# Kernel optimization log

Hardware: AMD Instinct MI355X
Metric: run time of the kernel (lower is better)

The kernel has to match this reference:

```python
import jax, jax.numpy as jnp
import numpy as np

N_NODES = 4096
N_EDGES = 131072  # avg degree 32
N_STEPS = 1000


def setup_inputs() -> dict:
    key = jax.random.key(0)
    k1, k2, k3 = jax.random.split(key, 3)
    # Transition matrices: positive entries so the evidence division is well-conditioned.
    Qt = jax.random.uniform(k1, (N_STEPS, 2, 2), minval=0.1, maxval=1.0, dtype=jnp.float32)
    edge_index_x_t = jax.random.randint(k2, (2, N_EDGES), 0, N_NODES)
    edge_index_x_start = jax.random.randint(k3, (2, N_EDGES), 0, N_NODES)
    return {
        "Qt": Qt,
        "edge_index_x_t": edge_index_x_t,
        "edge_index_x_start": edge_index_x_start,
        "t": 500,
        "num_nodes": N_NODES,
    }


def _edge_index_to_adj(edge_index, num_nodes):
    # Dense binary adjacency, matching torch edge_index_to_adj.
    adj = jnp.zeros((num_nodes, num_nodes), dtype=jnp.int32)
    return adj.at[edge_index[0], edge_index[1]].set(1)


def reference(Qt, edge_index_x_t, edge_index_x_start, t, num_nodes):
    # q(x_{t-1} | x_t, x_0) = (Q0[:, x_t] * Q_{t-1}[x_0, :]) / Q_t[x_0, x_t]
    Q_likelihood = Qt[0]        # (2, 2)
    Q_prior = Qt[t - 1]         # (2, 2)  (batch of 1 identical time)
    Q_evidence = Qt[t]          # (2, 2)

    adj_x_t = _edge_index_to_adj(edge_index_x_t, num_nodes)      # (N, N) in {0,1}
    adj_x_start = _edge_index_to_adj(edge_index_x_start, num_nodes)

    # likelihood[i,j,k] = Q_likelihood[k, adj_x_t[i,j]]
    likelihood = jnp.transpose(Q_likelihood[:, adj_x_t], (1, 2, 0))  # (N, N, 2)
    # prior[i,j,:] = Q_prior[adj_x_start[i,j], :]
    prior = Q_prior[adj_x_start]                                     # (N, N, 2)
    # evidence[i,j] = Q_evidence[adj_x_start[i,j], adj_x_t[i,j]]
    evidence = Q_evidence[adj_x_start, adj_x_t][..., None]           # (N, N, 1)

    q_backward = likelihood * prior / evidence                       # (N, N, 2)

    # block_diag of a single triu(N,N,diag=1) mask == upper triangle (all possible edges)
    iu, ju = jnp.triu_indices(num_nodes, k=1)
    # forward returns q_backward_all[:, 1]
    return q_backward[iu, ju, 1]                                     # (N*(N-1)/2,)
```

## Files before the change

kernel.cpp:

```cpp
#include <hip/hip_runtime.h>
#include <cstdint>

#define N_NODES 4096
#define N_EDGES 131072
#define OUT_QUADS (N_NODES * (N_NODES - 1) / 2 / 4)

__device__ __forceinline__ void compute_vals(const float* __restrict__ Qt,
                                             const int* __restrict__ t_ptr,
                                             float* vals) {
    const int t = t_ptr[0];
    const float l0 = Qt[2], l1 = Qt[3];
    const float p0 = Qt[(t - 1) * 4 + 1], p1 = Qt[(t - 1) * 4 + 3];
    const float e00 = Qt[t * 4 + 0], e01 = Qt[t * 4 + 1];
    const float e10 = Qt[t * 4 + 2], e11 = Qt[t * 4 + 3];
    float v0 = l0 * p0 / e00;
    float v1 = l1 * p0 / e01;
    float v2 = l0 * p1 / e10;
    float v3 = l1 * p1 / e11;
    uint32_t u0 = __float_as_uint(v0) & ~1u;
    uint32_t u1 = __float_as_uint(v1) |  1u;
    uint32_t u2 = __float_as_uint(v2) & ~1u;
    uint32_t u3 = __float_as_uint(v3) |  1u;
    vals[0] = __uint_as_float(u0);
    vals[1] = __uint_as_float(u1);
    vals[2] = __uint_as_float(u2);
    vals[3] = __uint_as_float(u3);
}

__device__ __forceinline__ int tri_idx(int i, int j) {
    return i * (2 * N_NODES - i - 1) / 2 + (j - i - 1);
}

__global__ void gt_fill_default(const float* __restrict__ Qt,
                                const int* __restrict__ t_ptr,
                                float4* __restrict__ out) {
    float vals[4];
    compute_vals(Qt, t_ptr, vals);
    const float4 v = make_float4(vals[0], vals[0], vals[0], vals[0]);
    int idx = blockIdx.x * blockDim.x + threadIdx.x;
    out[idx] = v;
}

__global__ void gt_scatter_t(const float* __restrict__ Qt,
                             const int* __restrict__ t_ptr,
                             const int* __restrict__ et,
                             float* __restrict__ out) {
    float vals[4];
    compute_vals(Qt, t_ptr, vals);
    int e = blockIdx.x * blockDim.x + threadIdx.x;
    int i = et[e];
    int j = et[N_EDGES + e];
    if (i < j) out[tri_idx(i, j)] = vals[1];
}

__global__ void gt_scatter_s(const float* __restrict__ Qt,
                             const int* __restrict__ t_ptr,
                             const int* __restrict__ es,
                             float* __restrict__ out) {
    float vals[4];
    compute_vals(Qt, t_ptr, vals);
    int e = blockIdx.x * blockDim.x + threadIdx.x;
    int i = es[e];
    int j = es[N_EDGES + e];
    if (i < j) {
        int idx = tri_idx(i, j);
        uint32_t cur = __float_as_uint(out[idx]);
        out[idx] = (cur & 1u) ? vals[3] : vals[2];
    }
}

extern "C" void kernel_launch(void* const* d_in, const int* in_sizes, int n_in,
                              void* d_out, int out_size, void* d_ws, size_t ws_size,
                              hipStream_t stream) {
    const float* Qt = (const float*)d_in[0];
    const int* et = (const int*)d_in[1];
    const int* es = (const int*)d_in[2];
    const int* t_ptr = (const int*)d_in[3];
    float* out = (float*)d_out;

    gt_fill_default<<<OUT_QUADS / 256, 256, 0, stream>>>(Qt, t_ptr, (float4*)out);
    gt_scatter_t<<<N_EDGES / 256, 256, 0, stream>>>(Qt, t_ptr, et, out);
    gt_scatter_s<<<N_EDGES / 256, 256, 0, stream>>>(Qt, t_ptr, es, out);
}
```

Before: 81.74 us.

## Build adjacency bitmaps with atomics then write output in one dense pass

The old approach filled the whole ~33MB output and then scattered edge values in two passes, the second pass reading back the output. The new version first builds two bitmaps in workspace, one per edge list, using atomicOr over the packed upper-triangle index. A single dense kernel then reads both bitmaps and writes each output quad from the four precomputed values. This drops the random read-modify-write scatters over the output. In exchange it adds a memset, an atomic bitmap pass and a bitmap read.

```diff
diff --git a/kernel.cpp b/kernel.cpp
--- a/kernel.cpp
+++ b/kernel.cpp
@@ -3,7 +3,9 @@
 
 #define N_NODES 4096
 #define N_EDGES 131072
-#define OUT_QUADS (N_NODES * (N_NODES - 1) / 2 / 4)
+#define OUT_ELEMS (N_NODES * (N_NODES - 1) / 2)
+#define OUT_QUADS (OUT_ELEMS / 4)
+#define BM_WORDS_PAD 262144
 
 __device__ __forceinline__ void compute_vals(const float* __restrict__ Qt,
                                              const int* __restrict__ t_ptr,
@@ -13,60 +15,59 @@
     const float p0 = Qt[(t - 1) * 4 + 1], p1 = Qt[(t - 1) * 4 + 3];
     const float e00 = Qt[t * 4 + 0], e01 = Qt[t * 4 + 1];
     const float e10 = Qt[t * 4 + 2], e11 = Qt[t * 4 + 3];
-    float v0 = l0 * p0 / e00;
-    float v1 = l1 * p0 / e01;
-    float v2 = l0 * p1 / e10;
-    float v3 = l1 * p1 / e11;
-    uint32_t u0 = __float_as_uint(v0) & ~1u;
-    uint32_t u1 = __float_as_uint(v1) |  1u;
-    uint32_t u2 = __float_as_uint(v2) & ~1u;
-    uint32_t u3 = __float_as_uint(v3) |  1u;
-    vals[0] = __uint_as_float(u0);
-    vals[1] = __uint_as_float(u1);
-    vals[2] = __uint_as_float(u2);
-    vals[3] = __uint_as_float(u3);
+    vals[0] = l0 * p0 / e00;
+    vals[1] = l1 * p0 / e01;
+    vals[2] = l0 * p1 / e10;
+    vals[3] = l1 * p1 / e11;
 }
 
 __device__ __forceinline__ int tri_idx(int i, int j) {
     return i * (2 * N_NODES - i - 1) / 2 + (j - i - 1);
 }
 
-__global__ void gt_fill_default(const float* __restrict__ Qt,
-                                const int* __restrict__ t_ptr,
-                                float4* __restrict__ out) {
+__global__ void gt_build_bitmaps(const int* __restrict__ et,
+                                 const int* __restrict__ es,
+                                 uint32_t* __restrict__ bm) {
+    int e = blockIdx.x * blockDim.x + threadIdx.x;
+    const int* __restrict__ lst;
+    uint32_t* __restrict__ map;
+    if (e < N_EDGES) {
+        lst = et;
+        map = bm;
+    } else {
+        lst = es;
+        map = bm + BM_WORDS_PAD;
+        e -= N_EDGES;
+    }
+    int i = lst[e];
+    int j = lst[N_EDGES + e];
+    if (i < j) {
+        int k = tri_idx(i, j);
+        atomicOr(&map[k >> 5], 1u << (k & 31));
+    }
+}
+
+__global__ void gt_write(const float* __restrict__ Qt,
+                         const int* __restrict__ t_ptr,
+                         const uint32_t* __restrict__ bm,
+                         float4* __restrict__ out) {
     float vals[4];
     compute_vals(Qt, t_ptr, vals);
-    const float4 v = make_float4(vals[0], vals[0], vals[0], vals[0]);
-    int idx = blockIdx.x * blockDim.x + threadIdx.x;
-    out[idx] = v;
-}
 
-__global__ void gt_scatter_t(const float* __restrict__ Qt,
-                             const int* __restrict__ t_ptr,
-                             const int* __restrict__ et,
-                             float* __restrict__ out) {
-    float vals[4];
-    compute_vals(Qt, t_ptr, vals);
-    int e = blockIdx.x * blockDim.x + threadIdx.x;
-    int i = et[e];
-    int j = et[N_EDGES + e];
-    if (i < j) out[tri_idx(i, j)] = vals[1];
-}
+    int tid = blockIdx.x * blockDim.x + threadIdx.x;
+    int w = tid >> 3;
+    int sh = (tid & 7) * 4;
+    uint32_t wt = bm[w] >> sh;
+    uint32_t ws = bm[BM_WORDS_PAD + w] >> sh;
 
-__global__ void gt_scatter_s(const float* __restrict__ Qt,
-                             const int* __restrict__ t_ptr,
-                             const int* __restrict__ es,
-                             float* __restrict__ out) {
-    float vals[4];
-    compute_vals(Qt, t_ptr, vals);
-    int e = blockIdx.x * blockDim.x + threadIdx.x;
-    int i = es[e];
-    int j = es[N_EDGES + e];
-    if (i < j) {
-        int idx = tri_idx(i, j);
-        uint32_t cur = __float_as_uint(out[idx]);
-        out[idx] = (cur & 1u) ? vals[3] : vals[2];
+    float r[4];
+#pragma unroll
+    for (int k = 0; k < 4; ++k) {
+        bool bt = (wt >> k) & 1u;
+        bool bs = (ws >> k) & 1u;
+        r[k] = bs ? (bt ? vals[3] : vals[2]) : (bt ? vals[1] : vals[0]);
     }
+    out[tid] = make_float4(r[0], r[1], r[2], r[3]);
 }
 
 extern "C" void kernel_launch(void* const* d_in, const int* in_sizes, int n_in,
@@ -77,8 +78,9 @@
     const int* es = (const int*)d_in[2];
     const int* t_ptr = (const int*)d_in[3];
     float* out = (float*)d_out;
+    uint32_t* bm = (uint32_t*)d_ws;
 
-    gt_fill_default<<<OUT_QUADS / 256, 256, 0, stream>>>(Qt, t_ptr, (float4*)out);
-    gt_scatter_t<<<N_EDGES / 256, 256, 0, stream>>>(Qt, t_ptr, et, out);
-    gt_scatter_s<<<N_EDGES / 256, 256, 0, stream>>>(Qt, t_ptr, es, out);
+    hipMemsetAsync(bm, 0, 2 * BM_WORDS_PAD * sizeof(uint32_t), stream);
+    gt_build_bitmaps<<<(2 * N_EDGES) / 256, 256, 0, stream>>>(et, es, bm);
+    gt_write<<<OUT_QUADS / 256, 256, 0, stream>>>(Qt, t_ptr, bm, (float4*)out);
 }
```

New measurement: 83.70 us. +2.4%, slower.
